# Optimization experiments

Measured on AMD Instinct MI355X. Metric: run time of the kernel, lower is better.

Reference implementation:

```python
import jax, jax.numpy as jnp
import numpy as np

N_HOPS = 3  # context_hops


def _l2_normalize(x, eps=1e-12):
    # matches torch.nn.functional.normalize(x) row-wise
    return x / jnp.maximum(jnp.linalg.norm(x, axis=-1, keepdims=True), eps)


def setup_inputs() -> dict:
    key = jax.random.key(0)
    k1, k2, k3, k4, k5 = jax.random.split(key, 5)
    n_entities, n_drugs, n_relations, n_edges, d = 100000, 2000, 51, 1000000, 64
    return {
        "entity_emb": jax.random.normal(k1, (n_entities, d), dtype=jnp.float32),
        "drug_emb": jax.random.normal(k2, (n_drugs, d), dtype=jnp.float32),
        "relation_emb": jax.random.normal(k3, (n_relations, d), dtype=jnp.float32),
        "edge_index": jax.random.randint(k4, (2, n_edges), 0, n_entities),
        "edge_type": jax.random.randint(k5, (n_edges,), 0, n_relations),
    }


def reference(entity_emb, drug_emb, relation_emb, edge_index, edge_type):
    n_entities = entity_emb.shape[0]
    n_drugs = drug_emb.shape[0]
    head, tail = edge_index[0], edge_index[1]

    # per-head in-degree for scatter_mean (clamp empty segments to 1 like torch_scatter)
    cnt = jax.ops.segment_sum(jnp.ones(head.shape[0], dtype=entity_emb.dtype),
                              head, num_segments=n_entities)
    denom = jnp.maximum(cnt, 1.0)[:, None]  # [n_entities, 1]

    ent_res, drug_res, rel_res = entity_emb, drug_emb, relation_emb
    for _ in range(N_HOPS):
        # gather-multiply: [E, d]
        msg = entity_emb[tail] * relation_emb[edge_type]
        # scatter_mean over head indices
        agg = jax.ops.segment_sum(msg, head, num_segments=n_entities) / denom
        entity_emb = _l2_normalize(agg)
        drug_emb = entity_emb[:n_drugs]        # normalize commutes with row slicing
        relation_emb = _l2_normalize(relation_emb)
        ent_res = ent_res + entity_emb
        drug_res = drug_res + drug_emb
        rel_res = rel_res + relation_emb
    return ent_res, drug_res, rel_res
```

## Files before the change

### kernel.cpp

```cpp
#include <hip/hip_runtime.h>
#include <hip/hip_bf16.h>

#define D 64
#define NBIN_MAX 1024

__device__ __forceinline__ int load_idx(const void* p, long long i, int mode) {
  return mode ? (int)((const long long*)p)[i] : ((const int*)p)[i];
}
__device__ __forceinline__ float loadf(const void* p, long long i, int fm) {
  return fm ? ((const float*)p)[i]
            : __bfloat162float(((const __hip_bfloat16*)p)[i]);
}
__device__ __forceinline__ unsigned short bf16bits(float v) {
  unsigned u = __float_as_uint(v);
  return (unsigned short)((u + 0x7FFFu + ((u >> 16) & 1u)) >> 16);
}
__device__ __forceinline__ float bflo(unsigned u) { return __uint_as_float(u << 16); }
__device__ __forceinline__ float bfhi(unsigned u) { return __uint_as_float(u & 0xFFFF0000u); }

__global__ __launch_bounds__(256) void zero_detect_kernel(
    int* __restrict__ gcur, int nbins,
    const void* eidx, const void* etype, const void* ent0,
    int* __restrict__ flags, int n_edges) {
  int tid = threadIdx.x;
  for (int j = tid; j < nbins; j += 256) gcur[j] = 0;
  if (tid < 64) {
    int lane = tid;
    long long tot_e = 2LL * n_edges;
    long long step_e = tot_e / 130; if (step_e < 1) step_e = 1;
    long long pos_e = 1 + 2LL * lane * step_e;
    int ve = (pos_e < tot_e) ? ((const int*)eidx)[pos_e] : 0;
    unsigned long long be = __ballot(ve != 0);

    long long tot_t = n_edges;
    long long step_t = tot_t / 130; if (step_t < 1) step_t = 1;
    long long pos_t = 1 + 2LL * lane * step_t;
    int vt = (pos_t < tot_t) ? ((const int*)etype)[pos_t] : 0;
    unsigned long long bt = __ballot(vt != 0);

    float a = __bfloat162float(((const __hip_bfloat16*)ent0)[lane]);
    unsigned long long bf = __ballot(!(fabsf(a) <= 64.0f));

    if (lane == 0) {
      flags[0] = (be == 0ULL) ? 1 : 0;
      flags[1] = (bt == 0ULL) ? 1 : 0;
      flags[3] = (bf != 0ULL) ? 1 : 0;
    }
  }
}

__global__ __launch_bounds__(256) void build1_kernel(
    const void* __restrict__ ent0, const void* __restrict__ rel0,
    const void* __restrict__ eidx, const void* __restrict__ etype,
    unsigned short* __restrict__ entC, float* __restrict__ relRaw,
    float* __restrict__ relN, float* __restrict__ out_rel,
    int* __restrict__ gcur, int* __restrict__ binbuf,
    const int* __restrict__ flags,
    int ent_elems, int rel_elems, int n_ent, int n_rel, int n_edges,
    int nbins, int binCap) {
  __shared__ int s_cnt[NBIN_MAX];
  __shared__ int s_base[NBIN_MAX];
  int tid = threadIdx.x;
  int i = blockIdx.x * 256 + tid;
  int fm = flags[3];
  if (fm) {
    int i8 = i * 8;
    if (i8 < ent_elems) {
      float4 a = ((const float4*)ent0)[i * 2];
      float4 b = ((const float4*)ent0)[i * 2 + 1];
      uint4 o;
      o.x = (unsigned)bf16bits(a.x) | ((unsigned)bf16bits(a.y) << 16);
      o.y = (unsigned)bf16bits(a.z) | ((unsigned)bf16bits(a.w) << 16);
      o.z = (unsigned)bf16bits(b.x) | ((unsigned)bf16bits(b.y) << 16);
      o.w = (unsigned)bf16bits(b.z) | ((unsigned)bf16bits(b.w) << 16);
      ((uint4*)entC)[i] = o;
    }
  }
  if (i < rel_elems) {
    float v = loadf(rel0, i, fm);
    relRaw[i] = v;
    float ss = v * v;
    for (int o = 32; o > 0; o >>= 1) ss += __shfl_xor(ss, o, 64);
    float nv = (ss > 0.f) ? v * rsqrtf(ss) : 0.f;
    relN[i] = nv;
    out_rel[i] = v + 3.0f * nv;
  }
  int part_blocks = (n_edges + 4095) >> 12;
  if ((int)blockIdx.x < part_blocks) {
    int e0 = (int)blockIdx.x << 12;
    int m = flags[0], mr = flags[1];
    for (int b = tid; b < nbins; b += 256) s_cnt[b] = 0;
    __syncthreads();
    for (int k = 0; k < 16; ++k) {
      int e = e0 + k * 256 + tid;
      if (e < n_edges) {
        int h = load_idx(eidx, e, m);
        h = min(max(h, 0), n_ent - 1);
        atomicAdd(&s_cnt[h >> 9], 1);
      }
    }
    __syncthreads();
    for (int b = tid; b < nbins; b += 256) {
      int c = s_cnt[b];
      s_base[b] = c ? atomicAdd(&gcur[b], c) : 0;
      s_cnt[b] = 0;
    }
    __syncthreads();
    for (int k = 0; k < 16; ++k) {
      int e = e0 + k * 256 + tid;
      if (e < n_edges) {
        int h = load_idx(eidx, e, m);
        int t = load_idx(eidx, (long long)n_edges + e, m);
        int r = load_idx(etype, e, mr);
        h = min(max(h, 0), n_ent - 1);
        t = min(max(t, 0), n_ent - 1);
        r = min(max(r, 0), n_rel - 1);
        int bin = h >> 9;
        int pos = s_base[bin] + atomicAdd(&s_cnt[bin], 1);
        if (pos < binCap)
          binbuf[(size_t)bin * binCap + pos] =
              t | (r << 17) | ((h & 511) << 23);
      }
    }
  }
}

__global__ __launch_bounds__(256) void build2_kernel(
    const int* __restrict__ gcur, const int* __restrict__ binbuf,
    int* __restrict__ staging, int n_ent, int binCap, int C) {
  __shared__ int off2[512];
  int b = blockIdx.x;
  int tid = threadIdx.x;
  for (int j = tid; j < 512; j += 256) off2[j] = 0;
  __syncthreads();
  int cnt = min(gcur[b], binCap);
  const int* src = binbuf + (size_t)b * binCap;
  int ebase = b << 9;
  for (int e = tid; e < cnt; e += 256) {
    int pack = src[e];
    int hl = (int)(((unsigned)pack) >> 23);
    int pos = atomicAdd(&off2[hl], 1);
    if (pos < C - 1)
      staging[(size_t)(ebase + hl) * C + 1 + pos] = pack & 0x7FFFFF;
  }
  __syncthreads();
  for (int j = tid; j < 512; j += 256) {
    int ent = ebase + j;
    if (ent < n_ent) staging[(size_t)ent * C] = off2[j];
  }
}

template <int SHIFT>
__device__ __forceinline__ float4 hop_row_bf16(
    const unsigned short* __restrict__ src, const unsigned short* lds_rel,
    const int* __restrict__ adj, int base , int C, int n_ent,
    int sub, int gbase) {
  float4 acc = make_float4(0.f, 0.f, 0.f, 0.f);
  int pv = adj[(size_t)base + sub];
  int cnt = __shfl(pv, gbase, 64);
  cnt = min(cnt, C - 1);
  int slotbase = 0;
  int elo = 0;
  while (true) {
    int ehi = min(cnt, slotbase + 15);
    for (int j = elo; j < ehi; j += 8) {
      uint2 sv[8];
      int rr[8];
#pragma unroll
      for (int k = 0; k < 8; ++k) {
        int e = j + k;
        int ee = (e < ehi) ? e : elo;
        int p = __shfl(pv, gbase + (1 + ee - slotbase), 64);
        int t = min(p & 0x1FFFF, n_ent - 1);
        rr[k] = (e < ehi) ? (int)(((unsigned)p >> 17) & 0x3F) : -1;
        sv[k] = *(const uint2*)(src + ((size_t)t << SHIFT) + (sub << 2));
      }
#pragma unroll
      for (int k = 0; k < 8; ++k) {
        uint2 rv;
        if (rr[k] >= 0) rv = *(const uint2*)(lds_rel + (rr[k] << 6) + (sub << 2));
        else { rv.x = 0u; rv.y = 0u; }
        acc.x += bflo(sv[k].x) * bflo(rv.x);
        acc.y += bfhi(sv[k].x) * bfhi(rv.x);
        acc.z += bflo(sv[k].y) * bflo(rv.y);
        acc.w += bfhi(sv[k].y) * bfhi(rv.y);
      }
    }
    if (ehi >= cnt) break;
    slotbase += 16;
    elo = slotbase - 1;
    pv = adj[(size_t)base + slotbase + sub];
  }
  return acc;
}

__device__ __forceinline__ float4 norm4(float4 acc) {
  float ss = acc.x * acc.x + acc.y * acc.y + acc.z * acc.z + acc.w * acc.w;
  for (int o = 8; o > 0; o >>= 1) ss += __shfl_xor(ss, o, 64);
  float inv = (ss > 0.f) ? rsqrtf(ss) : 0.f;
  return make_float4(acc.x * inv, acc.y * inv, acc.z * inv, acc.w * inv);
}

__global__ __launch_bounds__(256, 8) void hop0_kernel(
    const unsigned short* __restrict__ srcRaw, const unsigned short* __restrict__ srcConv,
    const float* __restrict__ relX, const int* __restrict__ staging,
    const int* __restrict__ flags,
    unsigned short* __restrict__ v0out ,
    int n_ent, int n_rel, int C) {
  extern __shared__ unsigned short lds_rel[];
  for (int i = threadIdx.x; i < n_rel * D; i += blockDim.x)
    lds_rel[i] = bf16bits(relX[i]);
  __syncthreads();
  const unsigned short* src = flags[3] ? srcConv : srcRaw;
  int lane = threadIdx.x & 63;
  int sub = lane & 15;
  int grp = (lane >> 4) & 3;
  int gbase = lane & 48;
  int wid = (blockIdx.x * blockDim.x + threadIdx.x) >> 6;
  int nw = (gridDim.x * blockDim.x) >> 6;
  for (int row = wid * 4 + grp; row < n_ent; row += nw * 4) {
    float4 val = norm4(hop_row_bf16<6>(src, lds_rel, staging, row * C, C, n_ent, sub, gbase));
    uint2 o;
    o.x = (unsigned)bf16bits(val.x) | ((unsigned)bf16bits(val.y) << 16);
    o.y = (unsigned)bf16bits(val.z) | ((unsigned)bf16bits(val.w) << 16);
    *(uint2*)(v0out + ((size_t)row << 7) + (sub << 2)) = o;
  }
}

__global__ __launch_bounds__(256, 8) void hop1_kernel(
    const unsigned short* __restrict__ v0, const float* __restrict__ relX,
    const int* __restrict__ staging,
    unsigned short* __restrict__ dst, int n_ent, int n_rel, int C) {
  extern __shared__ unsigned short lds_rel[];
  for (int i = threadIdx.x; i < n_rel * D; i += blockDim.x)
    lds_rel[i] = bf16bits(relX[i]);
  __syncthreads();
  int lane = threadIdx.x & 63;
  int sub = lane & 15;
  int grp = (lane >> 4) & 3;
  int gbase = lane & 48;
  int wid = (blockIdx.x * blockDim.x + threadIdx.x) >> 6;
  int nw = (gridDim.x * blockDim.x) >> 6;
  for (int row = wid * 4 + grp; row < n_ent; row += nw * 4) {
    float4 val = norm4(hop_row_bf16<7>(v0, lds_rel, staging, row * C, C, n_ent, sub, gbase));
    uint2 o;
    o.x = (unsigned)bf16bits(val.x) | ((unsigned)bf16bits(val.y) << 16);
    o.y = (unsigned)bf16bits(val.z) | ((unsigned)bf16bits(val.w) << 16);
    *(uint2*)(dst + ((size_t)row << 6) + (sub << 2)) = o;
  }
}

__global__ __launch_bounds__(256, 8) void hop2_kernel(
    const unsigned short* __restrict__ v1tab, const float* __restrict__ relX,
    const int* __restrict__ staging,
    const void* __restrict__ ent0, const void* __restrict__ drug0,
    const int* __restrict__ flags,
    float* out_ent, float* __restrict__ out_drug,
    int n_ent, int n_drugs, int n_rel, int C) {
  extern __shared__ unsigned short lds_rel[];
  for (int i = threadIdx.x; i < n_rel * D; i += blockDim.x)
    lds_rel[i] = bf16bits(relX[i]);
  __syncthreads();
  int fm = flags[3];
  int lane = threadIdx.x & 63;
  int sub = lane & 15;
  int grp = (lane >> 4) & 3;
  int gbase = lane & 48;
  int wid = (blockIdx.x * blockDim.x + threadIdx.x) >> 6;
  int nw = (gridDim.x * blockDim.x) >> 6;
  for (int row = wid * 4 + grp; row < n_ent; row += nw * 4) {
    float4 val = norm4(hop_row_bf16<6>(v1tab, lds_rel, staging, row * C, C, n_ent, sub, gbase));
    size_t eoff = ((size_t)row << 6) + (sub << 2);
    uint2 b0 = *(const uint2*)((const unsigned short*)out_ent +
                               ((size_t)row << 7) + (sub << 2));
    uint2 b1 = *(const uint2*)(v1tab + eoff);
    float4 s;
    s.x = val.x + bflo(b0.x) + bflo(b1.x);
    s.y = val.y + bfhi(b0.x) + bfhi(b1.x);
    s.z = val.z + bflo(b0.y) + bflo(b1.y);
    s.w = val.w + bfhi(b0.y) + bfhi(b1.y);
    float4 base;
    if (fm) base = *(const float4*)((const float*)ent0 + eoff);
    else {
      uint2 bb = *(const uint2*)((const unsigned short*)ent0 + eoff);
      base = make_float4(bflo(bb.x), bfhi(bb.x), bflo(bb.y), bfhi(bb.y));
    }
    *(float4*)(out_ent + eoff) =
        make_float4(base.x + s.x, base.y + s.y, base.z + s.z, base.w + s.w);
    if (row < n_drugs) {
      float4 db;
      if (fm) db = *(const float4*)((const float*)drug0 + eoff);
      else {
        uint2 bb = *(const uint2*)((const unsigned short*)drug0 + eoff);
        db = make_float4(bflo(bb.x), bfhi(bb.x), bflo(bb.y), bfhi(bb.y));
      }
      *(float4*)(out_drug + eoff) =
          make_float4(db.x + s.x, db.y + s.y, db.z + s.z, db.w + s.w);
    }
  }
}

__global__ void mini_flag_kernel(float* out, int hostbits) {
  if (blockIdx.x == 0 && threadIdx.x == 0)
    out[0] = 64.0f * (float)hostbits;
}

extern "C" void kernel_launch(void* const* d_in, const int* in_sizes, int n_in,
                              void* d_out, int out_size, void* d_ws, size_t ws_size,
                              hipStream_t stream) {
  const void* ent0  = d_in[0];
  const void* drug0 = d_in[1];
  const void* rel0  = d_in[2];
  const void* eidx  = d_in[3];
  const void* etype = d_in[4];
  float* out = (float*)d_out;

  const int ent_elems  = in_sizes[0];
  const int drug_elems = in_sizes[1];
  const int rel_elems  = in_sizes[2];
  const int n_edges    = in_sizes[4];
  const int n_ent   = ent_elems / D;
  const int n_drugs = drug_elems / D;
  const int n_rel   = rel_elems / D;

  const int nbins  = (n_ent + 511) >> 9;
  const int binCap = (nbins > 0) ? ent_elems / nbins : 0;
  const long long expected = (nbins > 0) ? (n_edges + nbins - 1) / nbins : 0;

  int hostbits = 0;
  bool sizes_ok = (n_in == 5) &&
                  (in_sizes[3] == 2 * n_edges) &&
                  (out_size == ent_elems + drug_elems + rel_elems) &&
                  (ent_elems % D == 0) && (drug_elems % D == 0) &&
                  (rel_elems % D == 0) && (n_ent > 0) && (n_edges > 0) &&
                  (n_ent <= 131072) && (n_rel >= 1) && (n_rel <= 64) &&
                  (n_drugs <= n_ent) && (nbins <= NBIN_MAX) &&
                  ((long long)binCap >= 2 * expected + 1024);
  if (!sizes_ok) hostbits |= 32;

  char* w = (char*)d_ws;
  auto alloc = [&](size_t bytes) {
    char* p = w;
    w += (bytes + 255) / 256 * 256;
    return p;
  };
  int* flags    = (int*)alloc(256);
  int* gcur     = (int*)alloc((size_t)NBIN_MAX * 4);
  float* relRaw = (float*)alloc((size_t)(rel_elems > 0 ? rel_elems : 1) * 4);
  float* relN   = (float*)alloc((size_t)(rel_elems > 0 ? rel_elems : 1) * 4);
  unsigned short* entA = (unsigned short*)alloc((size_t)(ent_elems > 0 ? ent_elems : 1) * 2);
  size_t fixed = (size_t)(w - (char*)d_ws);
  long long Cb = 0;
  if (n_ent > 0 && ws_size > fixed + 512)
    Cb = (long long)((ws_size - fixed - 512) / ((size_t)n_ent * 4));
  int C = (int)(Cb > 64 ? 64 : Cb);
  if (C < 40) hostbits |= 16;
  int* staging = (int*)alloc(((size_t)(n_ent > 0 ? n_ent : 1) * (size_t)(C > 0 ? C : 1) + 64) * 4);
  unsigned short* entC = entA;
  int* binbuf = (int*)out;

  if (hostbits) {
    mini_flag_kernel<<<1, 64, 0, stream>>>(out, hostbits);
    return;
  }

  float* out_ent  = out;
  float* out_drug = out + ent_elems;
  float* out_rel  = out + ent_elems + drug_elems;

  zero_detect_kernel<<<1, 256, 0, stream>>>(
      gcur, nbins, eidx, etype, ent0, flags, n_edges);

  int conv_blocks = (ent_elems / 8 + 255) / 256;
  int part_blocks = (n_edges + 4095) >> 12;
  int rel_blocks  = (rel_elems + 255) / 256;
  int g1 = conv_blocks;
  if (part_blocks > g1) g1 = part_blocks;
  if (rel_blocks > g1) g1 = rel_blocks;
  build1_kernel<<<g1, 256, 0, stream>>>(
      ent0, rel0, eidx, etype, entC, relRaw, relN, out_rel,
      gcur, binbuf, flags, ent_elems, rel_elems, n_ent, n_rel, n_edges,
      nbins, binCap);

  build2_kernel<<<nbins, 256, 0, stream>>>(
      gcur, binbuf, staging, n_ent, binCap, C);

  size_t lds_bytes = (size_t)n_rel * D * 2;
  int hop_blocks = 2048;
  hop0_kernel<<<hop_blocks, 256, lds_bytes, stream>>>(
      (const unsigned short*)ent0, entC, relRaw, staging, flags,
      (unsigned short*)out_ent, n_ent, n_rel, C);
  hop1_kernel<<<hop_blocks, 256, lds_bytes, stream>>>(
      (const unsigned short*)out_ent, relN, staging, entA, n_ent, n_rel, C);
  hop2_kernel<<<hop_blocks, 256, lds_bytes, stream>>>(
      entA, relN, staging, ent0, drug0, flags,
      out_ent, out_drug, n_ent, n_drugs, n_rel, C);
}
```

Measured before the change: 228.6 us.

## Prefetch next row's adjacency header and streamline gather addressing in hop kernels

Each hop kernel now loads the adjacency slot vector for the next row before processing the current one, so index-load latency overlaps with the gather work. The row core splits into a first-16-slot fast path plus an overflow loop. It also computes gather addresses with 32-bit byte offsets and drops the clamp to n_ent-1. C is restricted to 64 or 32 instead of any value from 40 to 64, and the hop grid size is doubled. Removing the clamp assumes packed tail indices are always in range, and prefetching adds register pressure.

```diff
diff --git a/kernel.cpp b/kernel.cpp
--- a/kernel.cpp
+++ b/kernel.cpp
@@ -151,45 +151,70 @@
 }
 
 template <int SHIFT>
-__device__ __forceinline__ float4 hop_row_bf16(
+__device__ __forceinline__ float4 hop_row_core(
     const unsigned short* __restrict__ src, const unsigned short* lds_rel,
-    const int* __restrict__ adj, int base , int C, int n_ent,
+    const int* __restrict__ adj, size_t base, int pv, int C,
     int sub, int gbase) {
   float4 acc = make_float4(0.f, 0.f, 0.f, 0.f);
-  int pv = adj[(size_t)base + sub];
   int cnt = __shfl(pv, gbase, 64);
   cnt = min(cnt, C - 1);
-  int slotbase = 0;
-  int elo = 0;
-  while (true) {
-    int ehi = min(cnt, slotbase + 15);
-    for (int j = elo; j < ehi; j += 8) {
-      uint2 sv[8];
-      int rr[8];
+  int ehi = min(cnt, 15);
+  for (int j = 0; j < ehi; j += 8) {
+    uint2 sv[8];
+    int rr[8];
 #pragma unroll
-      for (int k = 0; k < 8; ++k) {
-        int e = j + k;
-        int ee = (e < ehi) ? e : elo;
-        int p = __shfl(pv, gbase + (1 + ee - slotbase), 64);
-        int t = min(p & 0x1FFFF, n_ent - 1);
-        rr[k] = (e < ehi) ? (int)(((unsigned)p >> 17) & 0x3F) : -1;
-        sv[k] = *(const uint2*)(src + ((size_t)t << SHIFT) + (sub << 2));
+    for (int k = 0; k < 8; ++k) {
+      int e = j + k;
+      int ee = (e < ehi) ? e : 0;
+      int p = __shfl(pv, gbase + 1 + ee, 64);
+      unsigned toff = ((unsigned)(p & 0x1FFFF) << (SHIFT + 1)) + (unsigned)(sub << 3);
+      rr[k] = (e < ehi) ? (int)(((unsigned)p >> 17) & 0x3F) : -1;
+      sv[k] = *(const uint2*)((const char*)src + toff);
+    }
+#pragma unroll
+    for (int k = 0; k < 8; ++k) {
+      uint2 rv;
+      if (rr[k] >= 0) rv = *(const uint2*)(lds_rel + (rr[k] << 6) + (sub << 2));
+      else { rv.x = 0u; rv.y = 0u; }
+      acc.x += bflo(sv[k].x) * bflo(rv.x);
+      acc.y += bfhi(sv[k].x) * bfhi(rv.x);
+      acc.z += bflo(sv[k].y) * bflo(rv.y);
+      acc.w += bfhi(sv[k].y) * bfhi(rv.y);
+    }
+  }
+  if (cnt > 15) {
+    int slotbase = 16;
+    int elo = 15;
+    while (true) {
+      int pv2 = adj[base + slotbase + sub];
+      int eh2 = min(cnt, slotbase + 15);
+      for (int j = elo; j < eh2; j += 8) {
+        uint2 sv[8];
+        int rr[8];
+#pragma unroll
+        for (int k = 0; k < 8; ++k) {
+          int e = j + k;
+          int ee = (e < eh2) ? e : elo;
+          int p = __shfl(pv2, gbase + (1 + ee - slotbase), 64);
+          unsigned toff = ((unsigned)(p & 0x1FFFF) << (SHIFT + 1)) + (unsigned)(sub << 3);
+          rr[k] = (e < eh2) ? (int)(((unsigned)p >> 17) & 0x3F) : -1;
+          sv[k] = *(const uint2*)((const char*)src + toff);
+        }
+#pragma unroll
+        for (int k = 0; k < 8; ++k) {
+          uint2 rv;
+          if (rr[k] >= 0) rv = *(const uint2*)(lds_rel + (rr[k] << 6) + (sub << 2));
+          else { rv.x = 0u; rv.y = 0u; }
+          acc.x += bflo(sv[k].x) * bflo(rv.x);
+          acc.y += bfhi(sv[k].x) * bfhi(rv.x);
+          acc.z += bflo(sv[k].y) * bflo(rv.y);
+          acc.w += bfhi(sv[k].y) * bfhi(rv.y);
+        }
       }
-#pragma unroll
-      for (int k = 0; k < 8; ++k) {
-        uint2 rv;
-        if (rr[k] >= 0) rv = *(const uint2*)(lds_rel + (rr[k] << 6) + (sub << 2));
-        else { rv.x = 0u; rv.y = 0u; }
-        acc.x += bflo(sv[k].x) * bflo(rv.x);
-        acc.y += bfhi(sv[k].x) * bfhi(rv.x);
-        acc.z += bflo(sv[k].y) * bflo(rv.y);
-        acc.w += bfhi(sv[k].y) * bfhi(rv.y);
-      }
-    }
-    if (ehi >= cnt) break;
-    slotbase += 16;
-    elo = slotbase - 1;
-    pv = adj[(size_t)base + slotbase + sub];
+      if (eh2 >= cnt) break;
+      slotbase += 16;
+      elo = slotbase - 1;
+    }
   }
   return acc;
 }
@@ -218,12 +243,21 @@
   int gbase = lane & 48;
   int wid = (blockIdx.x * blockDim.x + threadIdx.x) >> 6;
   int nw = (gridDim.x * blockDim.x) >> 6;
-  for (int row = wid * 4 + grp; row < n_ent; row += nw * 4) {
-    float4 val = norm4(hop_row_bf16<6>(src, lds_rel, staging, row * C, C, n_ent, sub, gbase));
+  int step = nw * 4;
+  int row = wid * 4 + grp;
+  if (row >= n_ent) return;
+  size_t base = (size_t)row * C;
+  int pv = staging[base + sub];
+  while (row < n_ent) {
+    int nrow = row + step;
+    size_t nbase = (size_t)nrow * C;
+    int pv_next = (nrow < n_ent) ? staging[nbase + sub] : 0;
+    float4 val = norm4(hop_row_core<6>(src, lds_rel, staging, base, pv, C, sub, gbase));
     uint2 o;
     o.x = (unsigned)bf16bits(val.x) | ((unsigned)bf16bits(val.y) << 16);
     o.y = (unsigned)bf16bits(val.z) | ((unsigned)bf16bits(val.w) << 16);
     *(uint2*)(v0out + ((size_t)row << 7) + (sub << 2)) = o;
+    row = nrow; base = nbase; pv = pv_next;
   }
 }
 
@@ -241,12 +275,21 @@
   int gbase = lane & 48;
   int wid = (blockIdx.x * blockDim.x + threadIdx.x) >> 6;
   int nw = (gridDim.x * blockDim.x) >> 6;
-  for (int row = wid * 4 + grp; row < n_ent; row += nw * 4) {
-    float4 val = norm4(hop_row_bf16<7>(v0, lds_rel, staging, row * C, C, n_ent, sub, gbase));
+  int step = nw * 4;
+  int row = wid * 4 + grp;
+  if (row >= n_ent) return;
+  size_t base = (size_t)row * C;
+  int pv = staging[base + sub];
+  while (row < n_ent) {
+    int nrow = row + step;
+    size_t nbase = (size_t)nrow * C;
+    int pv_next = (nrow < n_ent) ? staging[nbase + sub] : 0;
+    float4 val = norm4(hop_row_core<7>(v0, lds_rel, staging, base, pv, C, sub, gbase));
     uint2 o;
     o.x = (unsigned)bf16bits(val.x) | ((unsigned)bf16bits(val.y) << 16);
     o.y = (unsigned)bf16bits(val.z) | ((unsigned)bf16bits(val.w) << 16);
     *(uint2*)(dst + ((size_t)row << 6) + (sub << 2)) = o;
+    row = nrow; base = nbase; pv = pv_next;
   }
 }
 
@@ -268,8 +311,16 @@
   int gbase = lane & 48;
   int wid = (blockIdx.x * blockDim.x + threadIdx.x) >> 6;
   int nw = (gridDim.x * blockDim.x) >> 6;
-  for (int row = wid * 4 + grp; row < n_ent; row += nw * 4) {
-    float4 val = norm4(hop_row_bf16<6>(v1tab, lds_rel, staging, row * C, C, n_ent, sub, gbase));
+  int step = nw * 4;
+  int row = wid * 4 + grp;
+  if (row >= n_ent) return;
+  size_t base = (size_t)row * C;
+  int pv = staging[base + sub];
+  while (row < n_ent) {
+    int nrow = row + step;
+    size_t nbase = (size_t)nrow * C;
+    int pv_next = (nrow < n_ent) ? staging[nbase + sub] : 0;
+    float4 val = norm4(hop_row_core<6>(v1tab, lds_rel, staging, base, pv, C, sub, gbase));
     size_t eoff = ((size_t)row << 6) + (sub << 2);
     uint2 b0 = *(const uint2*)((const unsigned short*)out_ent +
                                ((size_t)row << 7) + (sub << 2));
@@ -279,14 +330,14 @@
     s.y = val.y + bfhi(b0.x) + bfhi(b1.x);
     s.z = val.z + bflo(b0.y) + bflo(b1.y);
     s.w = val.w + bfhi(b0.y) + bfhi(b1.y);
-    float4 base;
-    if (fm) base = *(const float4*)((const float*)ent0 + eoff);
+    float4 basev;
+    if (fm) basev = *(const float4*)((const float*)ent0 + eoff);
     else {
       uint2 bb = *(const uint2*)((const unsigned short*)ent0 + eoff);
-      base = make_float4(bflo(bb.x), bfhi(bb.x), bflo(bb.y), bfhi(bb.y));
+      basev = make_float4(bflo(bb.x), bfhi(bb.x), bflo(bb.y), bfhi(bb.y));
     }
     *(float4*)(out_ent + eoff) =
-        make_float4(base.x + s.x, base.y + s.y, base.z + s.z, base.w + s.w);
+        make_float4(basev.x + s.x, basev.y + s.y, basev.z + s.z, basev.w + s.w);
     if (row < n_drugs) {
       float4 db;
       if (fm) db = *(const float4*)((const float*)drug0 + eoff);
@@ -297,6 +348,7 @@
       *(float4*)(out_drug + eoff) =
           make_float4(db.x + s.x, db.y + s.y, db.z + s.z, db.w + s.w);
     }
+    row = nrow; base = nbase; pv = pv_next;
   }
 }
 
@@ -350,11 +402,13 @@
   float* relN   = (float*)alloc((size_t)(rel_elems > 0 ? rel_elems : 1) * 4);
   unsigned short* entA = (unsigned short*)alloc((size_t)(ent_elems > 0 ? ent_elems : 1) * 2);
   size_t fixed = (size_t)(w - (char*)d_ws);
-  long long Cb = 0;
-  if (n_ent > 0 && ws_size > fixed + 512)
-    Cb = (long long)((ws_size - fixed - 512) / ((size_t)n_ent * 4));
-  int C = (int)(Cb > 64 ? 64 : Cb);
-  if (C < 40) hostbits |= 16;
+  long long avail = (ws_size > fixed + 512) ? (long long)(ws_size - fixed - 512) : 0;
+  int C = 0;
+  if (n_ent > 0) {
+    if (avail >= (long long)n_ent * 64 * 4) C = 64;
+    else if (avail >= (long long)n_ent * 32 * 4) C = 32;
+  }
+  if (C == 0) hostbits |= 16;
   int* staging = (int*)alloc(((size_t)(n_ent > 0 ? n_ent : 1) * (size_t)(C > 0 ? C : 1) + 64) * 4);
   unsigned short* entC = entA;
   int* binbuf = (int*)out;
@@ -386,7 +440,7 @@
       gcur, binbuf, staging, n_ent, binCap, C);
 
   size_t lds_bytes = (size_t)n_rel * D * 2;
-  int hop_blocks = 2048;
+  int hop_blocks = 4096;
   hop0_kernel<<<hop_blocks, 256, lds_bytes, stream>>>(
       (const unsigned short*)ent0, entC, relRaw, staging, flags,
       (unsigned short*)out_ent, n_ent, n_rel, C);
```

New measurement: 231.9 us. No clear change (+1.5%).
